# Optimization experiments

Measured on AMD Instinct MI355X. Metric: run time of the kernel, lower is better.

Reference implementation:

```python
import jax, jax.numpy as jnp
import numpy as np

# Grid config from init_kwargs
VX, VY = 0.1, 0.1
XMIN, YMIN, ZMIN, XMAX, YMAX, ZMAX = 0.0, -25.6, -3.0, 51.2, 25.6, 3.0
H = int(round((XMAX - XMIN) / VX))  # 512
W = int(round((YMAX - YMIN) / VY))  # 512
SIGMA = 1.5   # gaussian std in voxel units
R = 3         # splat window radius -> 7x7 kernel


def _pose0to1(pose0, pose1):
    # ego-motion: pose1^{-1} @ pose0, per batch element
    return jnp.linalg.inv(pose1) @ pose0


def _transform(xyz, pose):
    # xyz: [B,N,3], pose: [B,4,4] -> xyz @ R^T + t
    Rm = pose[:, :3, :3]
    t = pose[:, :3, 3]
    return jnp.einsum('bnd,bed->bne', xyz, Rm) + t[:, None, :]


def _voxelize(xyz):
    # continuous voxel coords + integer pillar indices + in-range mask
    px = (xyz[..., 0] - XMIN) / VX
    py = (xyz[..., 1] - YMIN) / VY
    ix = jnp.floor(px).astype(jnp.int32)
    iy = jnp.floor(py).astype(jnp.int32)
    valid = (ix >= 0) & (ix < H) & (iy >= 0) & (iy < W) & \
            (xyz[..., 2] >= ZMIN) & (xyz[..., 2] < ZMAX)
    return px, py, ix, iy, valid


def _gauss_heatmap(px, py, ix, iy, valid):
    # Splat a gaussian (max-composited) around every valid radar pillar.
    B, M = px.shape
    offs = jnp.arange(-R, R + 1)
    dx, dy = jnp.meshgrid(offs, offs, indexing='ij')      # [K,K]
    gx = ix[:, :, None, None] + dx                        # [B,M,K,K]
    gy = iy[:, :, None, None] + dy
    cellx = gx.astype(px.dtype) + 0.5
    celly = gy.astype(py.dtype) + 0.5
    d2 = (cellx - px[:, :, None, None]) ** 2 + (celly - py[:, :, None, None]) ** 2
    val = jnp.exp(-d2 / (2.0 * SIGMA * SIGMA))
    inb = (gx >= 0) & (gx < H) & (gy >= 0) & (gy < W) & valid[:, :, None, None]
    bidx = jnp.arange(B, dtype=jnp.int32)[:, None, None, None]
    flat = jnp.where(inb, bidx * (H * W) + gx * W + gy, B * H * W)  # dummy seg for invalid
    heat = jax.ops.segment_max(val.reshape(-1), flat.reshape(-1),
                               num_segments=B * H * W + 1)
    heat = jnp.maximum(heat[:B * H * W], 0.0).reshape(B, H, W)
    return heat


def _gather(heat, ix, iy, valid):
    # per-point gaussian score = heatmap at the point's pillar
    B = heat.shape[0]
    hf = heat.reshape(B, -1)
    idx = jnp.clip(ix, 0, H - 1) * W + jnp.clip(iy, 0, W - 1)
    s = jnp.take_along_axis(hf, idx, axis=1)
    return jnp.where(valid, s, 0.0)


def _forward(pc0, pc1, radar_pc0, radar_pc1, pose0, pose1):
    # pose computed under no_grad in the original -> stop_gradient
    pose_0to1 = jax.lax.stop_gradient(_pose0to1(pose0, pose1))
    tpc0 = _transform(pc0, pose_0to1)
    trad0_xyz = _transform(radar_pc0[..., :3], pose_0to1)
    # dynamic pillar voxelization (BEV coords)
    _, _, l0x, l0y, l0v = _voxelize(tpc0)
    _, _, l1x, l1y, l1v = _voxelize(pc1)
    r0px, r0py, r0x, r0y, r0v = _voxelize(trad0_xyz)
    r1px, r1py, r1x, r1y, r1v = _voxelize(radar_pc1[..., :3])
    # gaussian maps from radar pillars, scored for lidar + radar points
    heat0 = _gauss_heatmap(r0px, r0py, r0x, r0y, r0v)
    heat1 = _gauss_heatmap(r1px, r1py, r1x, r1y, r1v)
    lidar0 = _gather(heat0, l0x, l0y, l0v)   # [B,N]
    radar0 = _gather(heat0, r0x, r0y, r0v)   # [B,M]
    lidar1 = _gather(heat1, l1x, l1y, l1v)
    radar1 = _gather(heat1, r1x, r1y, r1v)
    return jnp.concatenate([lidar0, radar0, lidar1, radar1], axis=1)


def setup_inputs() -> dict:
    key = jax.random.key(0)
    ks = jax.random.split(key, 8)
    B, N, M = 8, 262144, 8192
    lo = jnp.array([XMIN, YMIN, ZMIN], dtype=jnp.float32)
    hi = jnp.array([XMAX, YMAX, ZMAX], dtype=jnp.float32)
    pc0 = jax.random.uniform(ks[0], (B, N, 3), dtype=jnp.float32) * (hi - lo) + lo
    pc1 = jax.random.uniform(ks[1], (B, N, 3), dtype=jnp.float32) * (hi - lo) + lo
    rxyz0 = jax.random.uniform(ks[2], (B, M, 3), dtype=jnp.float32) * (hi - lo) + lo
    rxyz1 = jax.random.uniform(ks[3], (B, M, 3), dtype=jnp.float32) * (hi - lo) + lo
    radar_pc0 = jnp.concatenate([rxyz0, jax.random.normal(ks[4], (B, M, 3), dtype=jnp.float32)], axis=-1)
    radar_pc1 = jnp.concatenate([rxyz1, jax.random.normal(ks[5], (B, M, 3), dtype=jnp.float32)], axis=-1)

    def mk_pose(k):
        t = jax.random.uniform(k, (B, 3), minval=-0.5, maxval=0.5, dtype=jnp.float32)
        eye = jnp.tile(jnp.eye(4, dtype=jnp.float32)[None], (B, 1, 1))
        return eye.at[:, :3, 3].set(t)

    pose0 = mk_pose(ks[6])
    pose1 = mk_pose(ks[7])
    return {"pc0": pc0, "pc1": pc1, "radar_pc0": radar_pc0,
            "radar_pc1": radar_pc1, "pose0": pose0, "pose1": pose1}


def reference(pc0, pc1, radar_pc0, radar_pc1, pose0, pose1):
    return _forward(pc0, pc1, radar_pc0, radar_pc1, pose0, pose1)
```

## Files before the change

### kernel.cpp

```cpp
#include <hip/hip_runtime.h>
#include <math.h>

#define GH 512
#define GW 512
#define GHW (GH * GW)
#define RR 3
#define TS 64
#define TSHIFT 6
#define TPB 8
#define NTILES (TPB * TPB)
#define CAP 1024


__device__ __forceinline__ void compute_pose(const float* __restrict__ P0,
                                             const float* __restrict__ P1,
                                             float* __restrict__ T) {
    double a00 = P1[0], a01 = P1[1], a02 = P1[2],  t1x = P1[3];
    double a10 = P1[4], a11 = P1[5], a12 = P1[6],  t1y = P1[7];
    double a20 = P1[8], a21 = P1[9], a22 = P1[10], t1z = P1[11];
    double c00 = a11 * a22 - a12 * a21;
    double c01 = a12 * a20 - a10 * a22;
    double c02 = a10 * a21 - a11 * a20;
    double det = a00 * c00 + a01 * c01 + a02 * c02;
    double id = 1.0 / det;
    double r00 = c00 * id;
    double r01 = (a02 * a21 - a01 * a22) * id;
    double r02 = (a01 * a12 - a02 * a11) * id;
    double r10 = c01 * id;
    double r11 = (a00 * a22 - a02 * a20) * id;
    double r12 = (a02 * a10 - a00 * a12) * id;
    double r20 = c02 * id;
    double r21 = (a01 * a20 - a00 * a21) * id;
    double r22 = (a00 * a11 - a01 * a10) * id;

    double b00 = P0[0], b01 = P0[1], b02 = P0[2],  t0x = P0[3];
    double b10 = P0[4], b11 = P0[5], b12 = P0[6],  t0y = P0[7];
    double b20 = P0[8], b21 = P0[9], b22 = P0[10], t0z = P0[11];
    double dx = t0x - t1x, dy = t0y - t1y, dz = t0z - t1z;

    T[0]  = (float)(r00 * b00 + r01 * b10 + r02 * b20);
    T[1]  = (float)(r00 * b01 + r01 * b11 + r02 * b21);
    T[2]  = (float)(r00 * b02 + r01 * b12 + r02 * b22);
    T[3]  = (float)(r00 * dx + r01 * dy + r02 * dz);
    T[4]  = (float)(r10 * b00 + r11 * b10 + r12 * b20);
    T[5]  = (float)(r10 * b01 + r11 * b11 + r12 * b21);
    T[6]  = (float)(r10 * b02 + r11 * b12 + r12 * b22);
    T[7]  = (float)(r10 * dx + r11 * dy + r12 * dz);
    T[8]  = (float)(r20 * b00 + r21 * b10 + r22 * b20);
    T[9]  = (float)(r20 * b01 + r21 * b11 + r22 * b21);
    T[10] = (float)(r20 * b02 + r21 * b12 + r22 * b22);
    T[11] = (float)(r20 * dx + r21 * dy + r22 * dz);
}

__device__ __forceinline__ void voxelize_xyz(float x, float y, float z,
                                             const float* __restrict__ T,
                                             float& px, float& py,
                                             int& ix, int& iy, bool& valid) {
    if (T) {
        float nx = T[0] * x + T[1] * y + T[2] * z + T[3];
        float ny = T[4] * x + T[5] * y + T[6] * z + T[7];
        float nz = T[8] * x + T[9] * y + T[10] * z + T[11];
        x = nx; y = ny; z = nz;
    }
    px = (x - 0.0f) * 10.0f;
    py = (y - (-25.6f)) * 10.0f;
    ix = (int)floorf(px);
    iy = (int)floorf(py);
    valid = (ix >= 0) & (ix < GH) & (iy >= 0) & (iy < GW) &
            (z >= -3.0f) & (z < 3.0f);
}

__global__ __launch_bounds__(256)
void heat_kernel(const float* __restrict__ radar0,
                 const float* __restrict__ radar1,
                 const float* __restrict__ pose0,
                 const float* __restrict__ pose1,
                 float* __restrict__ heat0,
                 float* __restrict__ heat1,
                 int B, int M) {
    __shared__ int tile[TS * TS];
    __shared__ float spx[CAP];
    __shared__ float spy[CAP];
    __shared__ float Tsh[12];
    __shared__ int sn;

    const int tid = threadIdx.x;
    const int blk = blockIdx.x;
    const int b = blk % B;
    const int map = (blk / B) & 1;
    const int tileIdx = blk / (2 * B);
    const int tx0 = (tileIdx >> 3) << TSHIFT;
    const int ty0 = (tileIdx & 7) << TSHIFT;

    if (tid == 0) {
        sn = 0;
        if (map == 0) compute_pose(pose0 + b * 16, pose1 + b * 16, Tsh);
    }
    for (int c = tid; c < TS * TS; c += 256) tile[c] = 0;
    __syncthreads();

    const float* radar = map ? radar1 : radar0;
    const float* T = map ? nullptr : Tsh;
    const float* pb = radar + (size_t)b * M * 6;

    for (int i = tid; i < M; i += 256) {
        const float* p = pb + (size_t)i * 6;
        float x = p[0], y = p[1], z = p[2];
        float px, py; int ix, iy; bool valid;
        voxelize_xyz(x, y, z, T, px, py, ix, iy, valid);
        if (!valid) continue;
        if (ix < tx0 - RR || ix > tx0 + TS - 1 + RR ||
            iy < ty0 - RR || iy > ty0 + TS - 1 + RR) continue;
        int slot = atomicAdd(&sn, 1);
        if (slot < CAP) { spx[slot] = px; spy[slot] = py; }
    }
    __syncthreads();

    int n = sn; if (n > CAP) n = CAP;
    const int total = n * 49;
    for (int t = tid; t < total; t += 256) {
        int pi = t / 49;
        int c = t - pi * 49;
        float px = spx[pi];
        float py = spy[pi];
        int ix = (int)floorf(px);
        int iy = (int)floorf(py);
        int dx = c / 7 - RR;
        int dy = c - (c / 7) * 7 - RR;
        int gx = ix + dx, gy = iy + dy;
        if (gx < tx0 || gx >= tx0 + TS || gy < ty0 || gy >= ty0 + TS) continue;
        float ddx = ((float)gx + 0.5f) - px;
        float ddy = ((float)gy + 0.5f) - py;
        float d2 = ddx * ddx + ddy * ddy;
        float val = expf(-d2 / 4.5f);
        atomicMax(&tile[(gx - tx0) * TS + (gy - ty0)], __float_as_int(val));
    }
    __syncthreads();

    float* heat = map ? heat1 : heat0;
    float* hb = heat + (size_t)b * GHW;
    for (int c4 = tid * 4; c4 < TS * TS; c4 += 1024) {
        int lx = c4 >> TSHIFT, ly = c4 & (TS - 1);
        int4 iv = *reinterpret_cast<const int4*>(&tile[c4]);
        float4 fv;
        fv.x = __int_as_float(iv.x);
        fv.y = __int_as_float(iv.y);
        fv.z = __int_as_float(iv.z);
        fv.w = __int_as_float(iv.w);
        *reinterpret_cast<float4*>(hb + (size_t)(tx0 + lx) * GW + (ty0 + ly)) = fv;
    }
}

__global__ __launch_bounds__(256)
void gather_fused_kernel(const float* __restrict__ pc0,
                         const float* __restrict__ pc1,
                         const float* __restrict__ radar0,
                         const float* __restrict__ radar1,
                         const float* __restrict__ pose0,
                         const float* __restrict__ pose1,
                         const float* __restrict__ heat0,
                         const float* __restrict__ heat1,
                         float* __restrict__ out,
                         int N, int M) {
    __shared__ float Tsh[12];
    const int row_len = 2 * N + 2 * M;
    const int b = blockIdx.x;
    const int base = blockIdx.y * 2048 + threadIdx.x;

    if (threadIdx.x == 0) compute_pose(pose0 + b * 16, pose1 + b * 16, Tsh);
    __syncthreads();

    const float* hb0 = heat0 + (size_t)b * GHW;
    const float* hb1 = heat1 + (size_t)b * GHW;
    const float* Tb = Tsh;

    float xs[8], ys[8], zs[8];
    const float* Ts[8];
    const float* hbs[8];
    bool live[8];

    #pragma unroll
    for (int k = 0; k < 8; k++) {
        int r = base + k * 256;
        live[k] = (r < row_len);
        if (!live[k]) continue;
        const float* p;
        const float* T = nullptr;
        const float* hb;
        if (r < N) {
            p = pc0 + ((size_t)b * N + r) * 3;
            T = Tb;
            hb = hb0;
        } else if (r < N + M) {
            p = radar0 + ((size_t)b * M + (r - N)) * 6;
            T = Tb;
            hb = hb0;
        } else if (r < 2 * N + M) {
            p = pc1 + ((size_t)b * N + (r - N - M)) * 3;
            hb = hb1;
        } else {
            p = radar1 + ((size_t)b * M + (r - 2 * N - M)) * 6;
            hb = hb1;
        }
        xs[k] = __builtin_nontemporal_load(p + 0);
        ys[k] = __builtin_nontemporal_load(p + 1);
        zs[k] = __builtin_nontemporal_load(p + 2);
        Ts[k] = T;
        hbs[k] = hb;
    }

    float v[8];
    #pragma unroll
    for (int k = 0; k < 8; k++) {
        if (!live[k]) continue;
        float px, py; int ix, iy; bool valid;
        voxelize_xyz(xs[k], ys[k], zs[k], Ts[k], px, py, ix, iy, valid);
        v[k] = 0.0f;
        if (valid) v[k] = hbs[k][ix * GW + iy];
    }

    #pragma unroll
    for (int k = 0; k < 8; k++) {
        if (!live[k]) continue;
        int r = base + k * 256;
        __builtin_nontemporal_store(v[k], out + (size_t)b * row_len + r);
    }
}

extern "C" void kernel_launch(void* const* d_in, const int* in_sizes, int n_in,
                              void* d_out, int out_size, void* d_ws, size_t ws_size,
                              hipStream_t stream) {
    const float* pc0      = (const float*)d_in[0];
    const float* pc1      = (const float*)d_in[1];
    const float* radar0   = (const float*)d_in[2];
    const float* radar1   = (const float*)d_in[3];
    const float* pose0    = (const float*)d_in[4];
    const float* pose1    = (const float*)d_in[5];
    float* out = (float*)d_out;

    int B = in_sizes[4] / 16;
    int N = in_sizes[0] / (B * 3);
    int M = in_sizes[2] / (B * 6);
    int row_len = 2 * N + 2 * M;

    float* heat0 = (float*)d_ws;
    float* heat1 = heat0 + (size_t)B * GHW;

    int nblk = 2 * B * NTILES;
    heat_kernel<<<nblk, 256, 0, stream>>>(
        radar0, radar1, pose0, pose1, heat0, heat1, B, M);

    dim3 ggrid(B, (row_len + 2047) / 2048);
    gather_fused_kernel<<<ggrid, 256, 0, stream>>>(
        pc0, pc1, radar0, radar1, pose0, pose1, heat0, heat1, out, N, M);
}
```

Before: 158.9 us.

## Fuse heatmap and gather into one cooperative kernel with global binning

```diff
diff --git a/kernel.cpp b/kernel.cpp
--- a/kernel.cpp
+++ b/kernel.cpp
@@ -1,5 +1,8 @@
 #include <hip/hip_runtime.h>
+#include <hip/hip_cooperative_groups.h>
 #include <math.h>
+
+namespace cg = cooperative_groups;
 
 #define GH 512
 #define GW 512
@@ -10,6 +13,7 @@
 #define TPB 8
 #define NTILES (TPB * TPB)
 #define CAP 1024
+#define NB 512
 
 
 __device__ __forceinline__ void compute_pose(const float* __restrict__ P0,
@@ -70,160 +74,175 @@
             (z >= -3.0f) & (z < 3.0f);
 }
 
-__global__ __launch_bounds__(256)
-void heat_kernel(const float* __restrict__ radar0,
-                 const float* __restrict__ radar1,
-                 const float* __restrict__ pose0,
-                 const float* __restrict__ pose1,
-                 float* __restrict__ heat0,
-                 float* __restrict__ heat1,
-                 int B, int M) {
+
+__global__ __launch_bounds__(256, 2)
+void fused_kernel(const float* __restrict__ pc0,
+                  const float* __restrict__ pc1,
+                  const float* __restrict__ radar0,
+                  const float* __restrict__ radar1,
+                  const float* __restrict__ pose0,
+                  const float* __restrict__ pose1,
+                  float* __restrict__ heat0,
+                  float* __restrict__ heat1,
+                  int* __restrict__ counts,
+                  float2* __restrict__ entries,
+                  float* __restrict__ out,
+                  int B, int N, int M) {
+    cg::grid_group grid = cg::this_grid();
+
     __shared__ int tile[TS * TS];
-    __shared__ float spx[CAP];
-    __shared__ float spy[CAP];
-    __shared__ float Tsh[12];
-    __shared__ int sn;
+    __shared__ float2 sp[CAP];
+    __shared__ float Tsh[8][12];
 
     const int tid = threadIdx.x;
     const int blk = blockIdx.x;
-    const int b = blk % B;
-    const int map = (blk / B) & 1;
-    const int tileIdx = blk / (2 * B);
-    const int tx0 = (tileIdx >> 3) << TSHIFT;
-    const int ty0 = (tileIdx & 7) << TSHIFT;
-
-    if (tid == 0) {
-        sn = 0;
-        if (map == 0) compute_pose(pose0 + b * 16, pose1 + b * 16, Tsh);
-    }
-    for (int c = tid; c < TS * TS; c += 256) tile[c] = 0;
-    __syncthreads();
-
-    const float* radar = map ? radar1 : radar0;
-    const float* T = map ? nullptr : Tsh;
-    const float* pb = radar + (size_t)b * M * 6;
-
-    for (int i = tid; i < M; i += 256) {
-        const float* p = pb + (size_t)i * 6;
-        float x = p[0], y = p[1], z = p[2];
+    const int nblk = gridDim.x;
+    const int BM = B * M;
+    const int nbins = 2 * B * NTILES;
+
+    if (tid < B) compute_pose(pose0 + tid * 16, pose1 + tid * 16, &Tsh[tid][0]);
+    for (int i = blk * 256 + tid; i < nbins; i += nblk * 256) counts[i] = 0;
+    grid.sync();
+
+    for (int t = blk * 256 + tid; t < 2 * BM; t += nblk * 256) {
+        int map = t / BM;
+        int rem = t - map * BM;
+        int b = rem / M;
+        const float* radar = map ? radar1 : radar0;
+        const float* T = map ? nullptr : &Tsh[b][0];
+        const float* p = radar + (size_t)rem * 6;
         float px, py; int ix, iy; bool valid;
-        voxelize_xyz(x, y, z, T, px, py, ix, iy, valid);
+        voxelize_xyz(p[0], p[1], p[2], T, px, py, ix, iy, valid);
         if (!valid) continue;
-        if (ix < tx0 - RR || ix > tx0 + TS - 1 + RR ||
-            iy < ty0 - RR || iy > ty0 + TS - 1 + RR) continue;
-        int slot = atomicAdd(&sn, 1);
-        if (slot < CAP) { spx[slot] = px; spy[slot] = py; }
-    }
-    __syncthreads();
-
-    int n = sn; if (n > CAP) n = CAP;
-    const int total = n * 49;
-    for (int t = tid; t < total; t += 256) {
-        int pi = t / 49;
-        int c = t - pi * 49;
-        float px = spx[pi];
-        float py = spy[pi];
-        int ix = (int)floorf(px);
-        int iy = (int)floorf(py);
-        int dx = c / 7 - RR;
-        int dy = c - (c / 7) * 7 - RR;
-        int gx = ix + dx, gy = iy + dy;
-        if (gx < tx0 || gx >= tx0 + TS || gy < ty0 || gy >= ty0 + TS) continue;
-        float ddx = ((float)gx + 0.5f) - px;
-        float ddy = ((float)gy + 0.5f) - py;
-        float d2 = ddx * ddx + ddy * ddy;
-        float val = expf(-d2 / 4.5f);
-        atomicMax(&tile[(gx - tx0) * TS + (gy - ty0)], __float_as_int(val));
-    }
-    __syncthreads();
-
-    float* heat = map ? heat1 : heat0;
-    float* hb = heat + (size_t)b * GHW;
-    for (int c4 = tid * 4; c4 < TS * TS; c4 += 1024) {
-        int lx = c4 >> TSHIFT, ly = c4 & (TS - 1);
-        int4 iv = *reinterpret_cast<const int4*>(&tile[c4]);
-        float4 fv;
-        fv.x = __int_as_float(iv.x);
-        fv.y = __int_as_float(iv.y);
-        fv.z = __int_as_float(iv.z);
-        fv.w = __int_as_float(iv.w);
-        *reinterpret_cast<float4*>(hb + (size_t)(tx0 + lx) * GW + (ty0 + ly)) = fv;
-    }
-}
-
-__global__ __launch_bounds__(256)
-void gather_fused_kernel(const float* __restrict__ pc0,
-                         const float* __restrict__ pc1,
-                         const float* __restrict__ radar0,
-                         const float* __restrict__ radar1,
-                         const float* __restrict__ pose0,
-                         const float* __restrict__ pose1,
-                         const float* __restrict__ heat0,
-                         const float* __restrict__ heat1,
-                         float* __restrict__ out,
-                         int N, int M) {
-    __shared__ float Tsh[12];
-    const int row_len = 2 * N + 2 * M;
-    const int b = blockIdx.x;
-    const int base = blockIdx.y * 2048 + threadIdx.x;
-
-    if (threadIdx.x == 0) compute_pose(pose0 + b * 16, pose1 + b * 16, Tsh);
-    __syncthreads();
-
-    const float* hb0 = heat0 + (size_t)b * GHW;
-    const float* hb1 = heat1 + (size_t)b * GHW;
-    const float* Tb = Tsh;
-
-    float xs[8], ys[8], zs[8];
-    const float* Ts[8];
-    const float* hbs[8];
-    bool live[8];
-
-    #pragma unroll
-    for (int k = 0; k < 8; k++) {
-        int r = base + k * 256;
-        live[k] = (r < row_len);
-        if (!live[k]) continue;
-        const float* p;
-        const float* T = nullptr;
-        const float* hb;
-        if (r < N) {
-            p = pc0 + ((size_t)b * N + r) * 3;
-            T = Tb;
-            hb = hb0;
-        } else if (r < N + M) {
-            p = radar0 + ((size_t)b * M + (r - N)) * 6;
-            T = Tb;
-            hb = hb0;
-        } else if (r < 2 * N + M) {
-            p = pc1 + ((size_t)b * N + (r - N - M)) * 3;
-            hb = hb1;
-        } else {
-            p = radar1 + ((size_t)b * M + (r - 2 * N - M)) * 6;
-            hb = hb1;
+        int txlo = max(ix - RR, 0) >> TSHIFT, txhi = min(ix + RR, GH - 1) >> TSHIFT;
+        int tylo = max(iy - RR, 0) >> TSHIFT, tyhi = min(iy + RR, GW - 1) >> TSHIFT;
+        for (int tx = txlo; tx <= txhi; tx++)
+            for (int ty = tylo; ty <= tyhi; ty++) {
+                int bin = (tx * TPB + ty) * (2 * B) + map * B + b;
+                int slot = atomicAdd(&counts[bin], 1);
+                if (slot < CAP)
+                    entries[(size_t)bin * CAP + slot] = make_float2(px, py);
+            }
+    }
+    grid.sync();
+
+    const int ntask = nbins;
+    for (int task = blk; task < ntask; task += nblk) {
+        int b = task % B;
+        int map = (task / B) & 1;
+        int tileIdx = task / (2 * B);
+        int tx0 = (tileIdx >> 3) << TSHIFT;
+        int ty0 = (tileIdx & 7) << TSHIFT;
+
+        int n = counts[task];
+        if (n > CAP) n = CAP;
+        const size_t base = (size_t)task * CAP;
+
+        for (int c = tid; c < TS * TS; c += 256) tile[c] = 0;
+        for (int i = tid; i < n; i += 256) sp[i] = entries[base + i];
+        __syncthreads();
+
+        const int total = n * 49;
+        for (int t = tid; t < total; t += 256) {
+            int pi = t / 49;
+            int c = t - pi * 49;
+            float px = sp[pi].x;
+            float py = sp[pi].y;
+            int ix = (int)floorf(px);
+            int iy = (int)floorf(py);
+            int dx = c / 7 - RR;
+            int dy = c - (c / 7) * 7 - RR;
+            int gx = ix + dx, gy = iy + dy;
+            if (gx < tx0 || gx >= tx0 + TS || gy < ty0 || gy >= ty0 + TS) continue;
+            float ddx = ((float)gx + 0.5f) - px;
+            float ddy = ((float)gy + 0.5f) - py;
+            float d2 = ddx * ddx + ddy * ddy;
+            float val = expf(-d2 / 4.5f);
+            atomicMax(&tile[(gx - tx0) * TS + (gy - ty0)], __float_as_int(val));
         }
-        xs[k] = __builtin_nontemporal_load(p + 0);
-        ys[k] = __builtin_nontemporal_load(p + 1);
-        zs[k] = __builtin_nontemporal_load(p + 2);
-        Ts[k] = T;
-        hbs[k] = hb;
-    }
-
-    float v[8];
-    #pragma unroll
-    for (int k = 0; k < 8; k++) {
-        if (!live[k]) continue;
-        float px, py; int ix, iy; bool valid;
-        voxelize_xyz(xs[k], ys[k], zs[k], Ts[k], px, py, ix, iy, valid);
-        v[k] = 0.0f;
-        if (valid) v[k] = hbs[k][ix * GW + iy];
-    }
-
-    #pragma unroll
-    for (int k = 0; k < 8; k++) {
-        if (!live[k]) continue;
-        int r = base + k * 256;
-        __builtin_nontemporal_store(v[k], out + (size_t)b * row_len + r);
+        __syncthreads();
+
+        float* heat = map ? heat1 : heat0;
+        float* hb = heat + (size_t)b * GHW;
+        for (int c4 = tid * 4; c4 < TS * TS; c4 += 1024) {
+            int lx = c4 >> TSHIFT, ly = c4 & (TS - 1);
+            int4 iv = *reinterpret_cast<const int4*>(&tile[c4]);
+            float4 fv;
+            fv.x = __int_as_float(iv.x);
+            fv.y = __int_as_float(iv.y);
+            fv.z = __int_as_float(iv.z);
+            fv.w = __int_as_float(iv.w);
+            *reinterpret_cast<float4*>(hb + (size_t)(tx0 + lx) * GW + (ty0 + ly)) = fv;
+        }
+        __syncthreads();
+    }
+    grid.sync();
+
+    {
+        const int row_len = 2 * N + 2 * M;
+        const int b = blk % B;
+        const int j = blk / B;
+        const int perb = nblk / B;
+        const int nchunk = (row_len + 2047) / 2048;
+        const float* hb0 = heat0 + (size_t)b * GHW;
+        const float* hb1 = heat1 + (size_t)b * GHW;
+        const float* Tb = &Tsh[b][0];
+
+        for (int ch = j; ch < nchunk; ch += perb) {
+            const int base2 = ch * 2048 + tid;
+
+            float xs[8], ys[8], zs[8];
+            const float* Ts[8];
+            const float* hbs[8];
+            bool live[8];
+
+            #pragma unroll
+            for (int k = 0; k < 8; k++) {
+                int r = base2 + k * 256;
+                live[k] = (r < row_len);
+                if (!live[k]) continue;
+                const float* p;
+                const float* T = nullptr;
+                const float* hb;
+                if (r < N) {
+                    p = pc0 + ((size_t)b * N + r) * 3;
+                    T = Tb;
+                    hb = hb0;
+                } else if (r < N + M) {
+                    p = radar0 + ((size_t)b * M + (r - N)) * 6;
+                    T = Tb;
+                    hb = hb0;
+                } else if (r < 2 * N + M) {
+                    p = pc1 + ((size_t)b * N + (r - N - M)) * 3;
+                    hb = hb1;
+                } else {
+                    p = radar1 + ((size_t)b * M + (r - 2 * N - M)) * 6;
+                    hb = hb1;
+                }
+                xs[k] = __builtin_nontemporal_load(p + 0);
+                ys[k] = __builtin_nontemporal_load(p + 1);
+                zs[k] = __builtin_nontemporal_load(p + 2);
+                Ts[k] = T;
+                hbs[k] = hb;
+            }
+
+            float v[8];
+            #pragma unroll
+            for (int k = 0; k < 8; k++) {
+                if (!live[k]) continue;
+                float px, py; int ix, iy; bool valid;
+                voxelize_xyz(xs[k], ys[k], zs[k], Ts[k], px, py, ix, iy, valid);
+                v[k] = 0.0f;
+                if (valid) v[k] = hbs[k][ix * GW + iy];
+            }
+
+            #pragma unroll
+            for (int k = 0; k < 8; k++) {
+                if (!live[k]) continue;
+                int r = base2 + k * 256;
+                __builtin_nontemporal_store(v[k], out + (size_t)b * row_len + r);
+            }
+        }
     }
 }
 
@@ -241,16 +260,20 @@
     int B = in_sizes[4] / 16;
     int N = in_sizes[0] / (B * 3);
     int M = in_sizes[2] / (B * 6);
-    int row_len = 2 * N + 2 * M;
+    int nbins = 2 * B * NTILES;
 
     float* heat0 = (float*)d_ws;
     float* heat1 = heat0 + (size_t)B * GHW;
-
-    int nblk = 2 * B * NTILES;
-    heat_kernel<<<nblk, 256, 0, stream>>>(
-        radar0, radar1, pose0, pose1, heat0, heat1, B, M);
-
-    dim3 ggrid(B, (row_len + 2047) / 2048);
-    gather_fused_kernel<<<ggrid, 256, 0, stream>>>(
-        pc0, pc1, radar0, radar1, pose0, pose1, heat0, heat1, out, N, M);
-}
+    float2* entries = (float2*)(heat1 + (size_t)B * GHW);
+    int* counts = (int*)(entries + (size_t)nbins * CAP);
+
+    void* args[] = {
+        (void*)&pc0, (void*)&pc1, (void*)&radar0, (void*)&radar1,
+        (void*)&pose0, (void*)&pose1,
+        (void*)&heat0, (void*)&heat1,
+        (void*)&counts, (void*)&entries,
+        (void*)&out, (void*)&B, (void*)&N, (void*)&M
+    };
+    hipLaunchCooperativeKernel((const void*)fused_kernel,
+                               dim3(NB), dim3(256), args, 0, stream);
+}
```

New measurement: 363.5 us. 129% more time.

## Replace 64x64 heatmap tiles with full-width 16-row strips

Applied to the files above, without the earlier changes.

```diff
diff --git a/kernel.cpp b/kernel.cpp
--- a/kernel.cpp
+++ b/kernel.cpp
@@ -5,11 +5,10 @@
 #define GW 512
 #define GHW (GH * GW)
 #define RR 3
-#define TS 64
-#define TSHIFT 6
-#define TPB 8
-#define NTILES (TPB * TPB)
-#define CAP 1024
+#define SH 16
+#define SSHIFT 4
+#define NSTRIP (GH / SH)
+#define SCAP 1024
 
 
 __device__ __forceinline__ void compute_pose(const float* __restrict__ P0,
@@ -71,16 +70,15 @@
 }
 
 __global__ __launch_bounds__(256)
-void heat_kernel(const float* __restrict__ radar0,
-                 const float* __restrict__ radar1,
-                 const float* __restrict__ pose0,
-                 const float* __restrict__ pose1,
-                 float* __restrict__ heat0,
-                 float* __restrict__ heat1,
-                 int B, int M) {
-    __shared__ int tile[TS * TS];
-    __shared__ float spx[CAP];
-    __shared__ float spy[CAP];
+void heat_strip_kernel(const float* __restrict__ radar0,
+                       const float* __restrict__ radar1,
+                       const float* __restrict__ pose0,
+                       const float* __restrict__ pose1,
+                       float* __restrict__ heat0,
+                       float* __restrict__ heat1,
+                       int B, int M) {
+    __shared__ int strip[SH * GW];
+    __shared__ float2 sp[SCAP];
     __shared__ float Tsh[12];
     __shared__ int sn;
 
@@ -88,66 +86,67 @@
     const int blk = blockIdx.x;
     const int b = blk % B;
     const int map = (blk / B) & 1;
-    const int tileIdx = blk / (2 * B);
-    const int tx0 = (tileIdx >> 3) << TSHIFT;
-    const int ty0 = (tileIdx & 7) << TSHIFT;
+    const int sx = blk / (2 * B);
+    const int x0 = sx << SSHIFT;
 
     if (tid == 0) {
         sn = 0;
         if (map == 0) compute_pose(pose0 + b * 16, pose1 + b * 16, Tsh);
     }
-    for (int c = tid; c < TS * TS; c += 256) tile[c] = 0;
+    {
+        const int4 z4 = make_int4(0, 0, 0, 0);
+        for (int c4 = tid * 4; c4 < SH * GW; c4 += 1024)
+            *reinterpret_cast<int4*>(&strip[c4]) = z4;
+    }
     __syncthreads();
 
     const float* radar = map ? radar1 : radar0;
     const float* T = map ? nullptr : Tsh;
-    const float* pb = radar + (size_t)b * M * 6;
+    const float2* pv = reinterpret_cast<const float2*>(radar + (size_t)b * M * 6);
 
     for (int i = tid; i < M; i += 256) {
-        const float* p = pb + (size_t)i * 6;
-        float x = p[0], y = p[1], z = p[2];
+        float2 fxy = pv[3 * i];
+        float2 fzw = pv[3 * i + 1];
         float px, py; int ix, iy; bool valid;
-        voxelize_xyz(x, y, z, T, px, py, ix, iy, valid);
+        voxelize_xyz(fxy.x, fxy.y, fzw.x, T, px, py, ix, iy, valid);
         if (!valid) continue;
-        if (ix < tx0 - RR || ix > tx0 + TS - 1 + RR ||
-            iy < ty0 - RR || iy > ty0 + TS - 1 + RR) continue;
+        if (ix < x0 - RR || ix > x0 + SH - 1 + RR) continue;
         int slot = atomicAdd(&sn, 1);
-        if (slot < CAP) { spx[slot] = px; spy[slot] = py; }
-    }
-    __syncthreads();
-
-    int n = sn; if (n > CAP) n = CAP;
+        if (slot < SCAP) sp[slot] = make_float2(px, py);
+    }
+    __syncthreads();
+
+    int n = sn; if (n > SCAP) n = SCAP;
     const int total = n * 49;
     for (int t = tid; t < total; t += 256) {
         int pi = t / 49;
         int c = t - pi * 49;
-        float px = spx[pi];
-        float py = spy[pi];
+        float px = sp[pi].x;
+        float py = sp[pi].y;
         int ix = (int)floorf(px);
         int iy = (int)floorf(py);
         int dx = c / 7 - RR;
         int dy = c - (c / 7) * 7 - RR;
         int gx = ix + dx, gy = iy + dy;
-        if (gx < tx0 || gx >= tx0 + TS || gy < ty0 || gy >= ty0 + TS) continue;
+        if (gx < x0 || gx >= x0 + SH || gy < 0 || gy >= GW) continue;
         float ddx = ((float)gx + 0.5f) - px;
         float ddy = ((float)gy + 0.5f) - py;
         float d2 = ddx * ddx + ddy * ddy;
         float val = expf(-d2 / 4.5f);
-        atomicMax(&tile[(gx - tx0) * TS + (gy - ty0)], __float_as_int(val));
+        atomicMax(&strip[(gx - x0) * GW + gy], __float_as_int(val));
     }
     __syncthreads();
 
     float* heat = map ? heat1 : heat0;
-    float* hb = heat + (size_t)b * GHW;
-    for (int c4 = tid * 4; c4 < TS * TS; c4 += 1024) {
-        int lx = c4 >> TSHIFT, ly = c4 & (TS - 1);
-        int4 iv = *reinterpret_cast<const int4*>(&tile[c4]);
+    float* hb = heat + (size_t)b * GHW + (size_t)x0 * GW;
+    for (int c4 = tid * 4; c4 < SH * GW; c4 += 1024) {
+        int4 iv = *reinterpret_cast<const int4*>(&strip[c4]);
         float4 fv;
         fv.x = __int_as_float(iv.x);
         fv.y = __int_as_float(iv.y);
         fv.z = __int_as_float(iv.z);
         fv.w = __int_as_float(iv.w);
-        *reinterpret_cast<float4*>(hb + (size_t)(tx0 + lx) * GW + (ty0 + ly)) = fv;
+        *reinterpret_cast<float4*>(hb + c4) = fv;
     }
 }
 
@@ -246,8 +245,8 @@
     float* heat0 = (float*)d_ws;
     float* heat1 = heat0 + (size_t)B * GHW;
 
-    int nblk = 2 * B * NTILES;
-    heat_kernel<<<nblk, 256, 0, stream>>>(
+    int nblk = 2 * B * NSTRIP;
+    heat_strip_kernel<<<nblk, 256, 0, stream>>>(
         radar0, radar1, pose0, pose1, heat0, heat1, B, M);
 
     dim3 ggrid(B, (row_len + 2047) / 2048);
```

After: 161.4 us. Within noise of the previous version (+1.6%).
